# Kernel optimization log

Hardware: AMD Instinct MI355X
Metric: run time of the kernel (lower is better)

Reference implementation:

```python
import jax, jax.numpy as jnp
import numpy as np

B, N, D = 2, 4096, 2048
H, DH, W = 8, 128, 512          # heads (num_queries), dim_head, window_size
SCALE = 8.0                      # qk_scale (qk_rmsnorm=True)


def setup_inputs() -> dict:
    key = jax.random.key(0)
    ks = jax.random.split(key, 5)
    return {
        "x": jax.random.normal(ks[0], (B, N, D), jnp.float32),
        "Wq": jax.random.normal(ks[1], (H * DH, D), jnp.float32) * 0.02,
        "Wkv": jax.random.normal(ks[2], (2 * H * DH, D), jnp.float32) * 0.02,
        "q_scale": jnp.ones((DH,), jnp.float32),
        "k_scale": jnp.ones((DH,), jnp.float32),
        "Wg": jax.random.normal(ks[3], (H, D), jnp.float32) * 0.02,
        "bg": jnp.zeros((H,), jnp.float32),
        "Wo": jax.random.normal(ks[4], (D, H * DH), jnp.float32) * 0.02,
    }


def _l2norm(t):
    # F.normalize: x / max(||x||, eps)
    return t / jnp.maximum(jnp.linalg.norm(t, axis=-1, keepdims=True), 1e-12)


def reference(x, Wq, Wkv, q_scale, k_scale, Wg, bg, Wo):
    b, n, _ = x.shape
    inner = H * DH
    q = (x @ Wq.T).reshape(b, n, H, DH).transpose(0, 2, 1, 3)      # b h n d
    kv = x @ Wkv.T
    k = kv[..., :inner].reshape(b, n, H, DH).transpose(0, 2, 1, 3)
    v = kv[..., inner:].reshape(b, n, H, DH).transpose(0, 2, 1, 3)
    # qk rmsnorm
    q = _l2norm(q) * q_scale
    k = _l2norm(k) * k_scale

    nb = n // W
    qb = q.reshape(b, H, nb, W, DH)
    kb = k.reshape(b, H, nb, W, DH)
    vb = v.reshape(b, H, nb, W, DH)

    def look_around(t):  # prepend previous bucket (look_backward=1)
        prev = jnp.concatenate([jnp.zeros_like(t[:, :, :1]), t[:, :, :-1]], axis=2)
        return jnp.concatenate([prev, t], axis=3)  # b h nb 2W d

    kw, vw = look_around(kb), look_around(vb)

    pos = jnp.arange(n).reshape(nb, W)
    pos_prev = jnp.concatenate([jnp.full((1, W), -1), pos[:-1]], axis=0)
    posk = jnp.concatenate([pos_prev, pos], axis=1)                 # nb 2W
    dist = pos[:, :, None] - posk[:, None, :]                       # nb W 2W
    # causal + exact window: attend j with 0 <= i - j <= W, valid (non-pad) key
    mask = (posk[:, None, :] >= 0) & (dist >= 0) & (dist <= W)

    sim = jnp.einsum('bhnid,bhnjd->bhnij', qb * SCALE, kw)
    sim = jnp.where(mask, sim, jnp.finfo(sim.dtype).min)
    attn = jax.nn.softmax(sim, axis=-1)
    o = jnp.einsum('bhnij,bhnjd->bhnid', attn, vw).reshape(b, H, n, DH)

    # per-head sigmoid value gating
    gates = jax.nn.sigmoid(jnp.einsum('bnd,hd->bhn', x, Wg) + bg[None, :, None])
    o = o * gates[..., None]

    o = o.transpose(0, 2, 1, 3).reshape(b, n, inner)                # b n (h d)
    return o @ Wo.T
```

## Files before the change

kernel.cpp:

```cpp
#include <hip/hip_runtime.h>
#include <hip/hip_bf16.h>
#include <cstdint>

typedef short short8 __attribute__((ext_vector_type(8)));
typedef short short4v __attribute__((ext_vector_type(4)));
typedef __bf16 bf16x8 __attribute__((ext_vector_type(8)));
typedef float f32x4 __attribute__((ext_vector_type(4)));
typedef unsigned short u16;
typedef unsigned int u32;

#define B_  2
#define N_  4096
#define D_  2048
#define H_  8
#define DH_ 128
#define W_  512
#define M_  (B_*N_)
#define INNER_ (H_*DH_)

static __device__ __forceinline__ u16 f2bf(float f) {
  u32 u = __float_as_uint(f);
  u32 r = (u + 0x7fffu + ((u >> 16) & 1u)) >> 16;
  return (u16)r;
}
static __device__ __forceinline__ float bf2f(u16 u) {
  return __uint_as_float(((u32)u) << 16);
}
static __device__ __forceinline__ f32x4 mfma16(short8 a, short8 b, f32x4 c) {
  return __builtin_amdgcn_mfma_f32_16x16x32_bf16(
      __builtin_bit_cast(bf16x8, a), __builtin_bit_cast(bf16x8, b), c, 0, 0, 0);
}

#define GLOAD_LDS16(g, s) \
  __builtin_amdgcn_global_load_lds((const __attribute__((address_space(1))) void*)(g), \
                                   (__attribute__((address_space(3))) void*)(s), 16, 0, 0)
#define BARRIER() __builtin_amdgcn_s_barrier()
#define SB0 __builtin_amdgcn_sched_barrier(0)
#define WVM4 asm volatile("s_waitcnt vmcnt(4)" ::: "memory")
#define WVM0 asm volatile("s_waitcnt vmcnt(0)" ::: "memory")

__global__ __launch_bounds__(256) void cvt_kernel(
    const float* __restrict__ x, const float* __restrict__ Wq,
    const float* __restrict__ Wkv, const float* __restrict__ Wo,
    u16* __restrict__ xb, u16* __restrict__ Wcat, u16* __restrict__ Wob) {
  size_t i = ((size_t)blockIdx.x * 256 + threadIdx.x) * 8;
  const float* src; u16* dst; size_t off;
  const size_t SX = 16777216ul, SQ = 2097152ul, SKV = 4194304ul;
  if (i < SX)                { src = x;   dst = xb;             off = i; }
  else if (i < SX+SQ)        { src = Wq;  dst = Wcat;           off = i - SX; }
  else if (i < SX+SQ+SKV)    { src = Wkv; dst = Wcat + 2097152; off = i - SX - SQ; }
  else                       { src = Wo;  dst = Wob;            off = i - SX - SQ - SKV; }
  float4 a = *(const float4*)(src + off);
  float4 b = *(const float4*)(src + off + 4);
  short8 o;
  o[0]=(short)f2bf(a.x); o[1]=(short)f2bf(a.y); o[2]=(short)f2bf(a.z); o[3]=(short)f2bf(a.w);
  o[4]=(short)f2bf(b.x); o[5]=(short)f2bf(b.y); o[6]=(short)f2bf(b.z); o[7]=(short)f2bf(b.w);
  *(short8*)(dst + off) = o;
}

template<int EPI>
__global__ __launch_bounds__(256) void gemm_bt(
    const u16* __restrict__ A, const u16* __restrict__ Bw,
    u16* __restrict__ Dst, float* __restrict__ Cf,
    const float* __restrict__ sc, int K) {
  __shared__ u16 sA[128*64];
  __shared__ u16 sB[128*64];
  __shared__ float pbuf[2][128];
  const int tid = threadIdx.x;
  const int lane = tid & 63, wv = tid >> 6;
  const int wm = wv >> 1, wn = wv & 1;
  const int m0 = blockIdx.y * 128, n0 = blockIdx.x * 128;
  const int l15 = lane & 15, l4 = lane >> 4;
  f32x4 acc[4][4] = {};

  #pragma unroll 1
  for (int kt = 0; kt < K; kt += 64) {
    __syncthreads();
    #pragma unroll
    for (int r = 0; r < 4; ++r) {
      int cf = r*256 + tid;
      int row = cf >> 3, cph = cf & 7;
      int clg = cph ^ (row & 7);
      GLOAD_LDS16(A + (size_t)(m0 + row)*K + kt + clg*8, sA + (size_t)(r*256 + wv*64)*8);
    }
    #pragma unroll
    for (int r = 0; r < 4; ++r) {
      int cf = r*256 + tid;
      int row = cf >> 3, cph = cf & 7;
      int clg = cph ^ (row & 7);
      GLOAD_LDS16(Bw + (size_t)(n0 + row)*K + kt + clg*8, sB + (size_t)(r*256 + wv*64)*8);
    }
    __syncthreads();
    #pragma unroll
    for (int ks = 0; ks < 2; ++ks) {
      short8 af[4], bfr[4];
      #pragma unroll
      for (int mf = 0; mf < 4; ++mf) {
        int row = wm*64 + mf*16 + l15;
        int ch = (ks*4 + l4) ^ (row & 7);
        af[mf] = *(const short8*)(sA + row*64 + ch*8);
      }
      #pragma unroll
      for (int nf = 0; nf < 4; ++nf) {
        int row = wn*64 + nf*16 + l15;
        int ch = (ks*4 + l4) ^ (row & 7);
        bfr[nf] = *(const short8*)(sB + row*64 + ch*8);
      }
      #pragma unroll
      for (int mf = 0; mf < 4; ++mf)
        #pragma unroll
        for (int nf = 0; nf < 4; ++nf)
          acc[mf][nf] = mfma16(af[mf], bfr[nf], acc[mf][nf]);
    }
  }

  if (EPI <= 1) {
    #pragma unroll
    for (int mf = 0; mf < 4; ++mf)
      #pragma unroll
      for (int j = 0; j < 4; ++j) {
        float ss = acc[mf][0][j]*acc[mf][0][j] + acc[mf][1][j]*acc[mf][1][j]
                 + acc[mf][2][j]*acc[mf][2][j] + acc[mf][3][j]*acc[mf][3][j];
        #pragma unroll
        for (int off = 1; off <= 8; off <<= 1) ss += __shfl_xor(ss, off);
        if (l15 == 0) pbuf[wn][wm*64 + mf*16 + l4*4 + j] = ss;
      }
    __syncthreads();
    const int h = blockIdx.x;
    const int b = m0 >> 12;
    #pragma unroll
    for (int mf = 0; mf < 4; ++mf)
      #pragma unroll
      for (int j = 0; j < 4; ++j) {
        int rloc = wm*64 + mf*16 + l4*4 + j;
        float ss = pbuf[0][rloc] + pbuf[1][rloc];
        float inv = 1.0f / fmaxf(sqrtf(ss), 1e-12f);
        if (EPI == 0) inv *= 8.0f;
        int n = (m0 + rloc) & (N_ - 1);
        size_t base = ((size_t)(b*H_ + h)*N_ + n) << 7;
        #pragma unroll
        for (int nf = 0; nf < 4; ++nf) {
          int d = wn*64 + nf*16 + l15;
          Dst[base + d] = f2bf(acc[mf][nf][j] * inv * sc[d]);
        }
      }
  } else if (EPI == 2) {
    const int h = blockIdx.x;
    const int b = m0 >> 12;
    const int bh = b*H_ + h;
    #pragma unroll
    for (int mf = 0; mf < 4; ++mf)
      #pragma unroll
      for (int nf = 0; nf < 4; ++nf) {
        int d = wn*64 + nf*16 + l15;
        int n = ((m0 & (N_ - 1)) + wm*64 + mf*16 + l4*4);
        short4v pk;
        pk[0] = (short)f2bf(acc[mf][nf][0]);
        pk[1] = (short)f2bf(acc[mf][nf][1]);
        pk[2] = (short)f2bf(acc[mf][nf][2]);
        pk[3] = (short)f2bf(acc[mf][nf][3]);
        *(short4v*)(Dst + ((size_t)bh*128 + d)*N_ + n) = pk;
      }
  } else {
    #pragma unroll
    for (int mf = 0; mf < 4; ++mf)
      #pragma unroll
      for (int nf = 0; nf < 4; ++nf)
        #pragma unroll
        for (int j = 0; j < 4; ++j) {
          int m = m0 + wm*64 + mf*16 + l4*4 + j;
          int nn = n0 + wn*64 + nf*16 + l15;
          Cf[(size_t)m*D_ + nn] = acc[mf][nf][j];
        }
  }
}

__global__ __launch_bounds__(256) void gates_kernel(
    const u16* __restrict__ xb, const float* __restrict__ Wg,
    const float* __restrict__ bg, float* __restrict__ gates) {
  int m = blockIdx.x;
  int tid = threadIdx.x;
  const u16* xr = xb + (size_t)m * D_;
  float acc[8] = {};
  for (int d0 = tid*8; d0 < D_; d0 += 256*8) {
    short8 xv8 = *(const short8*)(xr + d0);
    #pragma unroll
    for (int e = 0; e < 8; ++e) {
      float xv = bf2f((u16)xv8[e]);
      #pragma unroll
      for (int h = 0; h < 8; ++h) acc[h] = fmaf(xv, Wg[h*D_ + d0 + e], acc[h]);
    }
  }
  #pragma unroll
  for (int h = 0; h < 8; ++h)
    #pragma unroll
    for (int off = 32; off >= 1; off >>= 1) acc[h] += __shfl_xor(acc[h], off);
  __shared__ float red[4][8];
  int lane = tid & 63, wv = tid >> 6;
  if (lane == 0) {
    #pragma unroll
    for (int h = 0; h < 8; ++h) red[wv][h] = acc[h];
  }
  __syncthreads();
  if (tid < 8) {
    float vsum = red[0][tid] + red[1][tid] + red[2][tid] + red[3][tid] + bg[tid];
    gates[(size_t)m*8 + tid] = 1.0f / (1.0f + __expf(-vsum));
  }
}

__global__ __launch_bounds__(512, 4) void attn_kernel(
    const u16* __restrict__ q, const u16* __restrict__ k,
    const u16* __restrict__ vT, const float* __restrict__ gates,
    u16* __restrict__ o) {
  extern __shared__ u16 alds[];
  u16* sK = alds;
  u16* sV = alds + 16384;
  const int bid = blockIdx.x;
  const int t = bid & 3;
  const int c = (bid >> 2) & 7;
  const int bh = bid >> 5;
  const int b = bh >> 3, h = bh & 7;
  const int i0 = c*W_ + t*128;
  const int tid = threadIdx.x;
  const int lane = tid & 63, wv = tid >> 6;
  const int l15 = lane & 15, l4 = lane >> 4;
  u16* sPw = alds + 32768 + wv*1024;

#define STAGE_KV(KT, PB) do { \
    const int _j0 = i0 - 512 + (KT)*64; \
    u16* _dK = sK + (PB)*8192; \
    u16* _dV = sV + (PB)*8192; \
    _Pragma("unroll") for (int r = 0; r < 2; ++r) { \
      int cf = r*512 + tid; int row = cf >> 4, cph = cf & 15; \
      int clg = cph ^ (row & 15); \
      GLOAD_LDS16(k + (((size_t)bh*N_ + _j0 + row) << 7) + clg*8, _dK + (size_t)(r*512 + wv*64)*8); \
    } \
    _Pragma("unroll") for (int r = 0; r < 2; ++r) { \
      int cf = r*512 + tid; int row = cf >> 3, cph = cf & 7; \
      int clg = cph ^ (row & 7); \
      GLOAD_LDS16(vT + ((size_t)bh*128 + row)*N_ + _j0 + clg*8, _dV + (size_t)(r*512 + wv*64)*8); \
    } \
  } while(0)

  short8 qf[4];
  const u16* qbase = q + (((size_t)bh*N_ + i0 + wv*16) << 7);
  #pragma unroll
  for (int ks = 0; ks < 4; ++ks)
    qf[ks] = *(const short8*)(qbase + l15*128 + ks*32 + l4*8);

  float mrow[4], lrow[4];
  f32x4 oacc[8];
  #pragma unroll
  for (int j = 0; j < 4; ++j) { mrow[j] = -1e30f; lrow[j] = 0.f; }
  #pragma unroll
  for (int df = 0; df < 8; ++df) oacc[df] = (f32x4){0.f,0.f,0.f,0.f};

  const int kt0 = (i0 >= 512) ? 0 : ((512 - i0) >> 6);
  STAGE_KV(kt0, 0);

  #pragma unroll 1
  for (int kt = kt0; kt < 10; ++kt) {
    const int pb = (kt - kt0) & 1;
    if (kt < 9) { STAGE_KV(kt + 1, pb ^ 1); WVM4; } else { WVM0; }
    BARRIER(); SB0;

    const int base = 512 - kt*64;
    const int rmin = wv*16;
    if (base + rmin + 15 >= 0 && base + rmin - 63 <= 512) {
      const u16* cK = sK + pb*8192;
      const u16* cV = sV + pb*8192;

      f32x4 s[4];
      #pragma unroll
      for (int nf = 0; nf < 4; ++nf) s[nf] = (f32x4){0.f,0.f,0.f,0.f};
      #pragma unroll
      for (int ks = 0; ks < 4; ++ks) {
        short8 kb[4];
        #pragma unroll
        for (int nf = 0; nf < 4; ++nf) {
          int row = nf*16 + l15;
          int ch = (ks*4 + l4) ^ (row & 15);
          kb[nf] = *(const short8*)(cK + row*128 + ch*8);
        }
        #pragma unroll
        for (int nf = 0; nf < 4; ++nf)
          s[nf] = mfma16(qf[ks], kb[nf], s[nf]);
      }

      if (kt < 2 || kt > 7) {
        #pragma unroll
        for (int nf = 0; nf < 4; ++nf)
          #pragma unroll
          for (int j = 0; j < 4; ++j) {
            int r = rmin + l4*4 + j;
            int sidx = nf*16 + l15;
            int dist = base + r - sidx;
            if (dist < 0 || dist > 512) s[nf][j] = -1e30f;
          }
      }

      #pragma unroll
      for (int j = 0; j < 4; ++j) {
        float mx = fmaxf(fmaxf(s[0][j], s[1][j]), fmaxf(s[2][j], s[3][j]));
        #pragma unroll
        for (int off = 1; off <= 8; off <<= 1) mx = fmaxf(mx, __shfl_xor(mx, off));
        if (!__all(mx <= mrow[j] + 8.0f)) {
          float mnew = fmaxf(mrow[j], mx);
          float scal = __expf(mrow[j] - mnew);
          mrow[j] = mnew;
          lrow[j] *= scal;
          #pragma unroll
          for (int df = 0; df < 8; ++df) oacc[df][j] *= scal;
        }
        float m = mrow[j];
        float ls = 0.f;
        #pragma unroll
        for (int nf = 0; nf < 4; ++nf) {
          float p = __expf(s[nf][j] - m);
          s[nf][j] = p;
          ls += p;
        }
        #pragma unroll
        for (int off = 1; off <= 8; off <<= 1) ls += __shfl_xor(ls, off);
        lrow[j] += ls;
        int prow = l4*4 + j;
        #pragma unroll
        for (int nf = 0; nf < 4; ++nf) {
          int pcol = nf*16 + l15;
          int ch = (pcol >> 3) ^ (prow & 7);
          sPw[prow*64 + ch*8 + (pcol & 7)] = f2bf(s[nf][j]);
        }
      }

      #pragma unroll
      for (int ks2 = 0; ks2 < 2; ++ks2) {
        short8 pa;
        {
          int ch = (ks2*4 + l4) ^ (l15 & 7);
          pa = *(const short8*)(sPw + l15*64 + ch*8);
        }
        #pragma unroll
        for (int df = 0; df < 8; ++df) {
          int vd = df*16 + l15;
          int ch2 = (ks2*4 + l4) ^ (vd & 7);
          short8 vb = *(const short8*)(cV + vd*64 + ch2*8);
          oacc[df] = mfma16(pa, vb, oacc[df]);
        }
      }
    }
    BARRIER();
  }

  #pragma unroll
  for (int j = 0; j < 4; ++j) {
    int r = wv*16 + l4*4 + j;
    int i = i0 + r;
    float f = (1.0f / lrow[j]) * gates[((size_t)b*N_ + i)*8 + h];
    #pragma unroll
    for (int df = 0; df < 8; ++df)
      o[((size_t)b*N_ + i)*INNER_ + h*128 + df*16 + l15] = f2bf(oacc[df][j] * f);
  }
#undef STAGE_KV
}

extern "C" void kernel_launch(void* const* d_in, const int* in_sizes, int n_in,
                              void* d_out, int out_size, void* d_ws, size_t ws_size,
                              hipStream_t stream) {
  const float* x       = (const float*)d_in[0];
  const float* Wq      = (const float*)d_in[1];
  const float* Wkv     = (const float*)d_in[2];
  const float* q_scale = (const float*)d_in[3];
  const float* k_scale = (const float*)d_in[4];
  const float* Wg      = (const float*)d_in[5];
  const float* bg      = (const float*)d_in[6];
  const float* Wo      = (const float*)d_in[7];
  float* out = (float*)d_out;

  u16* qb  = (u16*)d_out;
  u16* kb  = qb + 8388608;
  u16* vTb = kb + 8388608;

  char* w = (char*)d_ws;
  u16* xb   = (u16*)w;
  u16* ob   = (u16*)w;
  u16* Wcat = (u16*)(w + 33554432);
  u16* Wob  = (u16*)(w + 46137344);
  float* gb = (float*)(w + 50331648);
  (void)in_sizes; (void)n_in; (void)out_size; (void)ws_size;

  hipFuncSetAttribute((const void*)attn_kernel,
                      hipFuncAttributeMaxDynamicSharedMemorySize, 81920);

  cvt_kernel<<<12288, 256, 0, stream>>>(x, Wq, Wkv, Wo, xb, Wcat, Wob);
  gemm_bt<0><<<dim3(8, 64), 256, 0, stream>>>(xb, Wcat,                       qb,  nullptr, q_scale, 2048);
  gemm_bt<1><<<dim3(8, 64), 256, 0, stream>>>(xb, Wcat + (size_t)1024*2048,   kb,  nullptr, k_scale, 2048);
  gemm_bt<2><<<dim3(8, 64), 256, 0, stream>>>(xb, Wcat + (size_t)2048*2048,   vTb, nullptr, nullptr, 2048);
  gates_kernel<<<8192, 256, 0, stream>>>(xb, Wg, bg, gb);
  attn_kernel<<<512, 512, 81920, stream>>>(qb, kb, vTb, gb, ob);
  gemm_bt<3><<<dim3(16, 64), 256, 0, stream>>>(ob, Wob, nullptr, out, nullptr, 1024);
}
```

Measured before the change: 288.7 us.

## Fuse Q/K/V projections into one GEMM launch with XCD-aware block swizzle

Merges the three separate Q, K and V projection GEMM launches into a single 1536-block kernel over the concatenated weight matrix. The output epilogue (normalized Q/K or transposed V) is selected per block from its column tile. Block indices are remapped so consecutive blocks sharing A rows land on the same XCD (index mod 8), for better L2 reuse of x and the weights; the output projection GEMM gets the same remap. This cuts launch overhead and tail effects from three small launches. It adds some divergent epilogue code in one kernel.

```diff
diff --git a/kernel.cpp b/kernel.cpp
--- a/kernel.cpp
+++ b/kernel.cpp
@@ -58,18 +58,20 @@
   *(short8*)(dst + off) = o;
 }
 
-template<int EPI>
-__global__ __launch_bounds__(256) void gemm_bt(
-    const u16* __restrict__ A, const u16* __restrict__ Bw,
-    u16* __restrict__ Dst, float* __restrict__ Cf,
-    const float* __restrict__ sc, int K) {
+__global__ __launch_bounds__(256) void gemm_qkv(
+    const u16* __restrict__ A, const u16* __restrict__ Wcat,
+    u16* __restrict__ Dq, u16* __restrict__ Dk, u16* __restrict__ Dv,
+    const float* __restrict__ qs, const float* __restrict__ ks) {
   __shared__ u16 sA[128*64];
   __shared__ u16 sB[128*64];
   __shared__ float pbuf[2][128];
+  const int K = D_;
+  const int s = (blockIdx.x & 7) * 192 + (blockIdx.x >> 3);
+  const int by = s / 24, bx = s % 24;
   const int tid = threadIdx.x;
   const int lane = tid & 63, wv = tid >> 6;
   const int wm = wv >> 1, wn = wv & 1;
-  const int m0 = blockIdx.y * 128, n0 = blockIdx.x * 128;
+  const int m0 = by * 128, n0 = bx * 128;
   const int l15 = lane & 15, l4 = lane >> 4;
   f32x4 acc[4][4] = {};
 
@@ -88,22 +90,22 @@
       int cf = r*256 + tid;
       int row = cf >> 3, cph = cf & 7;
       int clg = cph ^ (row & 7);
-      GLOAD_LDS16(Bw + (size_t)(n0 + row)*K + kt + clg*8, sB + (size_t)(r*256 + wv*64)*8);
+      GLOAD_LDS16(Wcat + (size_t)(n0 + row)*K + kt + clg*8, sB + (size_t)(r*256 + wv*64)*8);
     }
     __syncthreads();
     #pragma unroll
-    for (int ks = 0; ks < 2; ++ks) {
+    for (int ks2 = 0; ks2 < 2; ++ks2) {
       short8 af[4], bfr[4];
       #pragma unroll
       for (int mf = 0; mf < 4; ++mf) {
         int row = wm*64 + mf*16 + l15;
-        int ch = (ks*4 + l4) ^ (row & 7);
+        int ch = (ks2*4 + l4) ^ (row & 7);
         af[mf] = *(const short8*)(sA + row*64 + ch*8);
       }
       #pragma unroll
       for (int nf = 0; nf < 4; ++nf) {
         int row = wn*64 + nf*16 + l15;
-        int ch = (ks*4 + l4) ^ (row & 7);
+        int ch = (ks2*4 + l4) ^ (row & 7);
         bfr[nf] = *(const short8*)(sB + row*64 + ch*8);
       }
       #pragma unroll
@@ -114,7 +116,10 @@
     }
   }
 
-  if (EPI <= 1) {
+  const int sel = bx >> 3;
+  const int h = bx & 7;
+  const int b = m0 >> 12;
+  if (sel <= 1) {
     #pragma unroll
     for (int mf = 0; mf < 4; ++mf)
       #pragma unroll
@@ -126,8 +131,8 @@
         if (l15 == 0) pbuf[wn][wm*64 + mf*16 + l4*4 + j] = ss;
       }
     __syncthreads();
-    const int h = blockIdx.x;
-    const int b = m0 >> 12;
+    u16* dst = sel == 0 ? Dq : Dk;
+    const float* sc = sel == 0 ? qs : ks;
     #pragma unroll
     for (int mf = 0; mf < 4; ++mf)
       #pragma unroll
@@ -135,18 +140,16 @@
         int rloc = wm*64 + mf*16 + l4*4 + j;
         float ss = pbuf[0][rloc] + pbuf[1][rloc];
         float inv = 1.0f / fmaxf(sqrtf(ss), 1e-12f);
-        if (EPI == 0) inv *= 8.0f;
+        if (sel == 0) inv *= 8.0f;
         int n = (m0 + rloc) & (N_ - 1);
         size_t base = ((size_t)(b*H_ + h)*N_ + n) << 7;
         #pragma unroll
         for (int nf = 0; nf < 4; ++nf) {
           int d = wn*64 + nf*16 + l15;
-          Dst[base + d] = f2bf(acc[mf][nf][j] * inv * sc[d]);
-        }
-      }
-  } else if (EPI == 2) {
-    const int h = blockIdx.x;
-    const int b = m0 >> 12;
+          dst[base + d] = f2bf(acc[mf][nf][j] * inv * sc[d]);
+        }
+      }
+  } else {
     const int bh = b*H_ + h;
     #pragma unroll
     for (int mf = 0; mf < 4; ++mf)
@@ -159,20 +162,77 @@
         pk[1] = (short)f2bf(acc[mf][nf][1]);
         pk[2] = (short)f2bf(acc[mf][nf][2]);
         pk[3] = (short)f2bf(acc[mf][nf][3]);
-        *(short4v*)(Dst + ((size_t)bh*128 + d)*N_ + n) = pk;
-      }
-  } else {
-    #pragma unroll
-    for (int mf = 0; mf < 4; ++mf)
-      #pragma unroll
-      for (int nf = 0; nf < 4; ++nf)
-        #pragma unroll
-        for (int j = 0; j < 4; ++j) {
-          int m = m0 + wm*64 + mf*16 + l4*4 + j;
-          int nn = n0 + wn*64 + nf*16 + l15;
-          Cf[(size_t)m*D_ + nn] = acc[mf][nf][j];
-        }
-  }
+        *(short4v*)(Dv + ((size_t)bh*128 + d)*N_ + n) = pk;
+      }
+  }
+}
+
+__global__ __launch_bounds__(256) void gemm_proj(
+    const u16* __restrict__ A, const u16* __restrict__ Bw,
+    float* __restrict__ Cf) {
+  __shared__ u16 sA[128*64];
+  __shared__ u16 sB[128*64];
+  const int K = INNER_;
+  const int s = (blockIdx.x & 7) * 128 + (blockIdx.x >> 3);
+  const int by = s >> 4, bx = s & 15;
+  const int tid = threadIdx.x;
+  const int lane = tid & 63, wv = tid >> 6;
+  const int wm = wv >> 1, wn = wv & 1;
+  const int m0 = by * 128, n0 = bx * 128;
+  const int l15 = lane & 15, l4 = lane >> 4;
+  f32x4 acc[4][4] = {};
+
+  #pragma unroll 1
+  for (int kt = 0; kt < K; kt += 64) {
+    __syncthreads();
+    #pragma unroll
+    for (int r = 0; r < 4; ++r) {
+      int cf = r*256 + tid;
+      int row = cf >> 3, cph = cf & 7;
+      int clg = cph ^ (row & 7);
+      GLOAD_LDS16(A + (size_t)(m0 + row)*K + kt + clg*8, sA + (size_t)(r*256 + wv*64)*8);
+    }
+    #pragma unroll
+    for (int r = 0; r < 4; ++r) {
+      int cf = r*256 + tid;
+      int row = cf >> 3, cph = cf & 7;
+      int clg = cph ^ (row & 7);
+      GLOAD_LDS16(Bw + (size_t)(n0 + row)*K + kt + clg*8, sB + (size_t)(r*256 + wv*64)*8);
+    }
+    __syncthreads();
+    #pragma unroll
+    for (int ks2 = 0; ks2 < 2; ++ks2) {
+      short8 af[4], bfr[4];
+      #pragma unroll
+      for (int mf = 0; mf < 4; ++mf) {
+        int row = wm*64 + mf*16 + l15;
+        int ch = (ks2*4 + l4) ^ (row & 7);
+        af[mf] = *(const short8*)(sA + row*64 + ch*8);
+      }
+      #pragma unroll
+      for (int nf = 0; nf < 4; ++nf) {
+        int row = wn*64 + nf*16 + l15;
+        int ch = (ks2*4 + l4) ^ (row & 7);
+        bfr[nf] = *(const short8*)(sB + row*64 + ch*8);
+      }
+      #pragma unroll
+      for (int mf = 0; mf < 4; ++mf)
+        #pragma unroll
+        for (int nf = 0; nf < 4; ++nf)
+          acc[mf][nf] = mfma16(af[mf], bfr[nf], acc[mf][nf]);
+    }
+  }
+
+  #pragma unroll
+  for (int mf = 0; mf < 4; ++mf)
+    #pragma unroll
+    for (int nf = 0; nf < 4; ++nf)
+      #pragma unroll
+      for (int j = 0; j < 4; ++j) {
+        int m = m0 + wm*64 + mf*16 + l4*4 + j;
+        int nn = n0 + wn*64 + nf*16 + l15;
+        Cf[(size_t)m*D_ + nn] = acc[mf][nf][j];
+      }
 }
 
 __global__ __launch_bounds__(256) void gates_kernel(
@@ -392,10 +452,8 @@
                       hipFuncAttributeMaxDynamicSharedMemorySize, 81920);
 
   cvt_kernel<<<12288, 256, 0, stream>>>(x, Wq, Wkv, Wo, xb, Wcat, Wob);
-  gemm_bt<0><<<dim3(8, 64), 256, 0, stream>>>(xb, Wcat,                       qb,  nullptr, q_scale, 2048);
-  gemm_bt<1><<<dim3(8, 64), 256, 0, stream>>>(xb, Wcat + (size_t)1024*2048,   kb,  nullptr, k_scale, 2048);
-  gemm_bt<2><<<dim3(8, 64), 256, 0, stream>>>(xb, Wcat + (size_t)2048*2048,   vTb, nullptr, nullptr, 2048);
+  gemm_qkv<<<1536, 256, 0, stream>>>(xb, Wcat, qb, kb, vTb, q_scale, k_scale);
   gates_kernel<<<8192, 256, 0, stream>>>(xb, Wg, bg, gb);
   attn_kernel<<<512, 512, 81920, stream>>>(qb, kb, vTb, gb, ob);
-  gemm_bt<3><<<dim3(16, 64), 256, 0, stream>>>(ob, Wob, nullptr, out, nullptr, 1024);
-}
+  gemm_proj<<<1024, 256, 0, stream>>>(ob, Wob, out);
+}
```

After: 279.5 us. -3.2%, faster.

## Merge Q/K/V projections into one GEMM launch, move norm and V transpose to separate kernels

Applied to the files above, without the earlier changes.

The three separate projection GEMMs (Q, K, V with fused rmsnorm/transpose epilogues) are replaced by a single GEMM over the concatenated 3072-wide weight that writes raw bf16 Q, K, V in head-major layout. A new normqk kernel then applies the L2 normalization, scale and the x8 query factor in place, and a new tiled transpose kernel produces V^T for the attention kernel. The intent is to fill the GPU with one larger launch (1536 blocks instead of three of 512). The cost is extra global-memory round trips for Q/K normalization and the V transpose, an additional bf16 rounding of Q/K before normalization, and a wider buffer in the output scratch area.

```diff
diff --git a/kernel.cpp b/kernel.cpp
--- a/kernel.cpp
+++ b/kernel.cpp
@@ -61,11 +61,10 @@
 template<int EPI>
 __global__ __launch_bounds__(256) void gemm_bt(
     const u16* __restrict__ A, const u16* __restrict__ Bw,
-    u16* __restrict__ Dst, float* __restrict__ Cf,
-    const float* __restrict__ sc, int K) {
+    u16* __restrict__ Dq, u16* __restrict__ Dk, u16* __restrict__ Dv,
+    float* __restrict__ Cf, int N, int K) {
   __shared__ u16 sA[128*64];
   __shared__ u16 sB[128*64];
-  __shared__ float pbuf[2][128];
   const int tid = threadIdx.x;
   const int lane = tid & 63, wv = tid >> 6;
   const int wm = wv >> 1, wn = wv & 1;
@@ -114,53 +113,21 @@
     }
   }
 
-  if (EPI <= 1) {
+  if (EPI == 0) {
+    const int bufsel = blockIdx.x >> 3;
+    const int h = blockIdx.x & 7;
+    u16* dst = bufsel == 0 ? Dq : (bufsel == 1 ? Dk : Dv);
     #pragma unroll
     for (int mf = 0; mf < 4; ++mf)
       #pragma unroll
-      for (int j = 0; j < 4; ++j) {
-        float ss = acc[mf][0][j]*acc[mf][0][j] + acc[mf][1][j]*acc[mf][1][j]
-                 + acc[mf][2][j]*acc[mf][2][j] + acc[mf][3][j]*acc[mf][3][j];
-        #pragma unroll
-        for (int off = 1; off <= 8; off <<= 1) ss += __shfl_xor(ss, off);
-        if (l15 == 0) pbuf[wn][wm*64 + mf*16 + l4*4 + j] = ss;
-      }
-    __syncthreads();
-    const int h = blockIdx.x;
-    const int b = m0 >> 12;
-    #pragma unroll
-    for (int mf = 0; mf < 4; ++mf)
-      #pragma unroll
-      for (int j = 0; j < 4; ++j) {
-        int rloc = wm*64 + mf*16 + l4*4 + j;
-        float ss = pbuf[0][rloc] + pbuf[1][rloc];
-        float inv = 1.0f / fmaxf(sqrtf(ss), 1e-12f);
-        if (EPI == 0) inv *= 8.0f;
-        int n = (m0 + rloc) & (N_ - 1);
-        size_t base = ((size_t)(b*H_ + h)*N_ + n) << 7;
-        #pragma unroll
-        for (int nf = 0; nf < 4; ++nf) {
+      for (int nf = 0; nf < 4; ++nf)
+        #pragma unroll
+        for (int j = 0; j < 4; ++j) {
+          int m = m0 + wm*64 + mf*16 + l4*4 + j;
           int d = wn*64 + nf*16 + l15;
-          Dst[base + d] = f2bf(acc[mf][nf][j] * inv * sc[d]);
-        }
-      }
-  } else if (EPI == 2) {
-    const int h = blockIdx.x;
-    const int b = m0 >> 12;
-    const int bh = b*H_ + h;
-    #pragma unroll
-    for (int mf = 0; mf < 4; ++mf)
-      #pragma unroll
-      for (int nf = 0; nf < 4; ++nf) {
-        int d = wn*64 + nf*16 + l15;
-        int n = ((m0 & (N_ - 1)) + wm*64 + mf*16 + l4*4);
-        short4v pk;
-        pk[0] = (short)f2bf(acc[mf][nf][0]);
-        pk[1] = (short)f2bf(acc[mf][nf][1]);
-        pk[2] = (short)f2bf(acc[mf][nf][2]);
-        pk[3] = (short)f2bf(acc[mf][nf][3]);
-        *(short4v*)(Dst + ((size_t)bh*128 + d)*N_ + n) = pk;
-      }
+          int b = m >> 12, n = m & (N_ - 1);
+          dst[(((size_t)(b*H_ + h)*N_ + n) << 7) + d] = f2bf(acc[mf][nf][j]);
+        }
   } else {
     #pragma unroll
     for (int mf = 0; mf < 4; ++mf)
@@ -170,8 +137,53 @@
         for (int j = 0; j < 4; ++j) {
           int m = m0 + wm*64 + mf*16 + l4*4 + j;
           int nn = n0 + wn*64 + nf*16 + l15;
-          Cf[(size_t)m*D_ + nn] = acc[mf][nf][j];
-        }
+          Cf[(size_t)m*N + nn] = acc[mf][nf][j];
+        }
+  }
+}
+
+__global__ __launch_bounds__(256) void normqk_kernel(
+    u16* __restrict__ qb, u16* __restrict__ kb,
+    const float* __restrict__ qs, const float* __restrict__ ks) {
+  int lane = threadIdx.x & 63, wv = threadIdx.x >> 6;
+  size_t vec = (size_t)blockIdx.x * 4 + wv;
+  bool isq = vec < 65536;
+  u16* p = isq ? qb + vec*128 : kb + (vec - 65536)*128;
+  const float* sc = isq ? qs : ks;
+  u32 u = *(const u32*)(p + lane*2);
+  float a = bf2f((u16)(u & 0xffffu));
+  float b = bf2f((u16)(u >> 16));
+  float ss = a*a + b*b;
+  #pragma unroll
+  for (int off = 32; off >= 1; off >>= 1) ss += __shfl_xor(ss, off);
+  float inv = 1.0f / fmaxf(sqrtf(ss), 1e-12f);
+  if (isq) inv *= 8.0f;
+  float r0 = a * inv * sc[lane*2];
+  float r1 = b * inv * sc[lane*2 + 1];
+  *(u32*)(p + lane*2) = (u32)f2bf(r0) | ((u32)f2bf(r1) << 16);
+}
+
+__global__ __launch_bounds__(256) void transpose_v_kernel(
+    const u16* __restrict__ v, u16* __restrict__ vT) {
+  int bh = blockIdx.x >> 6;
+  int n0 = (blockIdx.x & 63) << 6;
+  __shared__ u16 tl[64][136];
+  int tid = threadIdx.x;
+  #pragma unroll
+  for (int r = 0; r < 4; ++r) {
+    int cf = r*256 + tid;
+    int row = cf >> 4, ch = cf & 15;
+    *(short8*)&tl[row][ch*8] = *(const short8*)(v + ((size_t)bh*N_ + n0 + row)*128 + ch*8);
+  }
+  __syncthreads();
+  #pragma unroll
+  for (int r = 0; r < 4; ++r) {
+    int cf = r*256 + tid;
+    int d = cf >> 3, nch = cf & 7;
+    short8 o;
+    #pragma unroll
+    for (int i = 0; i < 8; ++i) o[i] = (short)tl[nch*8 + i][d];
+    *(short8*)(vT + ((size_t)bh*128 + d)*N_ + n0 + nch*8) = o;
   }
 }
 
@@ -378,7 +390,8 @@
 
   u16* qb  = (u16*)d_out;
   u16* kb  = qb + 8388608;
-  u16* vTb = kb + 8388608;
+  u16* vb  = kb + 8388608;
+  u16* vTb = vb + 8388608;
 
   char* w = (char*)d_ws;
   u16* xb   = (u16*)w;
@@ -392,10 +405,10 @@
                       hipFuncAttributeMaxDynamicSharedMemorySize, 81920);
 
   cvt_kernel<<<12288, 256, 0, stream>>>(x, Wq, Wkv, Wo, xb, Wcat, Wob);
-  gemm_bt<0><<<dim3(8, 64), 256, 0, stream>>>(xb, Wcat,                       qb,  nullptr, q_scale, 2048);
-  gemm_bt<1><<<dim3(8, 64), 256, 0, stream>>>(xb, Wcat + (size_t)1024*2048,   kb,  nullptr, k_scale, 2048);
-  gemm_bt<2><<<dim3(8, 64), 256, 0, stream>>>(xb, Wcat + (size_t)2048*2048,   vTb, nullptr, nullptr, 2048);
+  gemm_bt<0><<<dim3(24, 64), 256, 0, stream>>>(xb, Wcat, qb, kb, vb, nullptr, 3072, 2048);
+  normqk_kernel<<<32768, 256, 0, stream>>>(qb, kb, q_scale, k_scale);
+  transpose_v_kernel<<<1024, 256, 0, stream>>>(vb, vTb);
   gates_kernel<<<8192, 256, 0, stream>>>(xb, Wg, bg, gb);
   attn_kernel<<<512, 512, 81920, stream>>>(qb, kb, vTb, gb, ob);
-  gemm_bt<3><<<dim3(16, 64), 256, 0, stream>>>(ob, Wob, nullptr, out, nullptr, 1024);
-}
+  gemm_bt<1><<<dim3(16, 64), 256, 0, stream>>>(ob, Wob, nullptr, nullptr, nullptr, out, 2048, 1024);
+}
```

Measured after the change: 286.4 us. About the same (-0.8%).
